# Kernel optimization log

Measured on AMD Instinct MI355X. Metric: run time of the kernel, lower is better.

## Reference

```python
import jax, jax.numpy as jnp
import numpy as np

B, T, C = 4, 2048, 1024
H = 16
HD = C // H


def setup_inputs() -> dict:
    key = jax.random.key(0)
    k1, k2, k3 = jax.random.split(key, 3)
    x = jax.random.normal(k1, (B, T, C), dtype=jnp.float32)
    w_qkv = jax.random.normal(k2, (C, 3 * C), dtype=jnp.float32) * (C ** -0.5)
    w_proj = jax.random.normal(k3, (C, C), dtype=jnp.float32) * (C ** -0.5)
    b_proj = jnp.zeros((C,), dtype=jnp.float32)
    return {"x": x, "w_qkv": w_qkv, "w_proj": w_proj, "b_proj": b_proj}


def reference(x, w_qkv, w_proj, b_proj):
    Bd, Td, Cd = x.shape
    scale = HD ** -0.5
    qkv = x @ w_qkv  # [B,T,3C]
    q, k, v = jnp.split(qkv, 3, axis=-1)
    # [B,H,T,HD]
    q = q.reshape(Bd, Td, H, HD).transpose(0, 2, 1, 3)
    k = k.reshape(Bd, Td, H, HD).transpose(0, 2, 1, 3)
    v = v.reshape(Bd, Td, H, HD).transpose(0, 2, 1, 3)
    att = jnp.einsum('bhqd,bhkd->bhqk', q, k) * scale
    causal = jnp.triu(jnp.ones((Td, Td), dtype=bool), k=1)
    att = jnp.where(causal, -jnp.inf, att)
    att = jax.nn.softmax(att, axis=-1)
    y = jnp.einsum('bhqk,bhkd->bhqd', att, v)
    y = y.transpose(0, 2, 1, 3).reshape(Bd, Td, Cd)
    return y @ w_proj + b_proj
```

## Files before the change

kernel.cpp:

```cpp
#include <hip/hip_runtime.h>

typedef unsigned short u16;
typedef __attribute__((ext_vector_type(8))) short short8;
typedef __attribute__((ext_vector_type(4))) short short4v;
typedef __attribute__((ext_vector_type(4))) float floatx4;
typedef __attribute__((ext_vector_type(4))) unsigned short ushort4v;

#define B_ 4
#define T_ 2048
#define C_ 1024
#define H_ 16
#define HD_ 64

template <bool V> struct BC { static constexpr bool value = V; };
template <int N> struct ICN { static constexpr int v = N; };

static __device__ __forceinline__ u16 f2bf(float f) {
  union { float f; unsigned int i; } c; c.f = f;
  unsigned int u = c.i;
  return (u16)((u + 0x7FFFu + ((u >> 16) & 1u)) >> 16);
}
static __device__ __forceinline__ unsigned pk2(float lo, float hi) {
  union { float f; unsigned u; } a, b; a.f = hi; b.f = lo;
  return __builtin_amdgcn_perm(a.u, b.u, 0x07060302u);
}
static __device__ __forceinline__ unsigned pk2r(float lo, float hi) {
  return (unsigned)f2bf(lo) | ((unsigned)f2bf(hi) << 16);
}

static __device__ __forceinline__ void gload16(const u16* g, u16* l) {
  __builtin_amdgcn_global_load_lds(
      (const __attribute__((address_space(1))) unsigned int*)(g),
      (__attribute__((address_space(3))) unsigned int*)(l), 16, 0, 0);
}

template <int N> static __device__ __forceinline__ void wait_vm_bar() {
  if constexpr (N == 6)
    asm volatile("s_waitcnt vmcnt(6)\n\ts_barrier" ::: "memory");
  else if constexpr (N == 4)
    asm volatile("s_waitcnt vmcnt(4)\n\ts_barrier" ::: "memory");
  else if constexpr (N == 0)
    asm volatile("s_waitcnt vmcnt(0)\n\ts_barrier" ::: "memory");
}

__global__ __launch_bounds__(256) void prep_k(const float* __restrict__ x,
                                              const float* __restrict__ w_qkv,
                                              const float* __restrict__ w_proj,
                                              u16* __restrict__ xbf,
                                              u16* __restrict__ wqkvT,
                                              u16* __restrict__ wprojT) {
  const int bid = blockIdx.x;
  if (bid < 8192) {
    const int i = bid * 256 + threadIdx.x;
    const float4 f = ((const float4*)x)[i];
    ushort4v o;
    o.x = f2bf(f.x); o.y = f2bf(f.y); o.z = f2bf(f.z); o.w = f2bf(f.w);
    *(ushort4v*)(xbf + (size_t)i * 4) = o;
    return;
  }
  __shared__ u16 tile[32][33];
  const float* in;
  u16* out;
  int R, Cc, tb;
  if (bid < 11264) {
    in = w_qkv; out = wqkvT; R = C_; Cc = 3 * C_; tb = bid - 8192;
  } else {
    in = w_proj; out = wprojT; R = C_; Cc = C_; tb = bid - 11264;
  }
  const int tpr = Cc / 32;
  const int bx = (tb % tpr) * 32;
  const int by = (tb / tpr) * 32;
  const int tx = threadIdx.x & 31;
  const int ty = threadIdx.x >> 5;
  #pragma unroll
  for (int i = ty; i < 32; i += 8)
    tile[i][tx] = f2bf(in[(size_t)(by + i) * Cc + bx + tx]);
  __syncthreads();
  #pragma unroll
  for (int i = ty; i < 32; i += 8)
    out[(size_t)(bx + i) * R + by + tx] = tile[tx][i];
}

template <int MODE, int NFR>
__global__ __launch_bounds__(256, 2) void gemm4w(const u16* __restrict__ A,
                                                 const u16* __restrict__ Bt,
                                                 u16* __restrict__ outb,
                                                 u16* __restrict__ outv,
                                                 float* __restrict__ outf,
                                                 const float* __restrict__ bias,
                                                 int M, int N) {
  constexpr int TN = NFR * 32;
  constexpr int BUFA = 4096;
  constexpr int BUFB = TN * 32;
  constexpr int BUF = BUFA + BUFB;
  constexpr int LPW = (8 + TN / 16) / 4;
  __shared__ __align__(16) u16 lds[3 * BUF];

  const int bid = blockIdx.x;
  const int xcd = bid & 7;
  const int loc = bid >> 3;
  const int tM = (xcd * 8 + (loc & 7)) * 128;
  const int tN = (loc >> 3) * TN;
  const int tid = threadIdx.x;
  const int wave = tid >> 6;
  const int lane = tid & 63;
  const int lr = lane & 15;
  const int quad = lane >> 4;
  const int wm = wave >> 1;
  const int wn = wave & 1;
  const int csw = (lr >> 1) & 3;
  const int srow = lane >> 2;
  const int skofs = ((lane & 3) ^ ((lane >> 3) & 3)) * 8;

  const u16* gbase[LPW];
  int ldst[LPW];
  #pragma unroll
  for (int j = 0; j < LPW; j++) {
    const int s = wave * LPW + j;
    if (s < 8) {
      gbase[j] = A + (size_t)(tM + s * 16 + srow) * 1024 + skofs;
      ldst[j] = s * 512;
    } else {
      gbase[j] = Bt + (size_t)(tN + (s - 8) * 16 + srow) * 1024 + skofs;
      ldst[j] = BUFA + (s - 8) * 512;
    }
  }

  const floatx4 zf = {0.f, 0.f, 0.f, 0.f};
  floatx4 acc[4][NFR];
  #pragma unroll
  for (int i = 0; i < 4; i++)
    #pragma unroll
    for (int j = 0; j < NFR; j++) acc[i][j] = zf;

  auto stage = [&](int t, int buf) {
    #pragma unroll
    for (int j = 0; j < LPW; j++)
      gload16(gbase[j] + t * 32, &lds[buf * BUF + ldst[j]]);
  };

  auto ktile = [&](int t, int buf, auto VM) {
    constexpr int vm = decltype(VM)::v;
    const u16* lA = &lds[buf * BUF];
    const u16* lB = lA + BUFA;
    short8 af[4], bfr[NFR];
    #pragma unroll
    for (int mt = 0; mt < 4; mt++)
      af[mt] = *(const short8*)(&lA[(wm * 64 + mt * 16 + lr) * 32 + ((quad ^ csw) * 8)]);
    #pragma unroll
    for (int nt = 0; nt < NFR; nt++)
      bfr[nt] = *(const short8*)(&lB[(wn * (NFR * 16) + nt * 16 + lr) * 32 + ((quad ^ csw) * 8)]);
    if constexpr (vm > 0) stage(t + 2, (buf + 2) % 3);
    __builtin_amdgcn_s_setprio(1);
    #pragma unroll
    for (int mt = 0; mt < 4; mt++)
      #pragma unroll
      for (int nt = 0; nt < NFR; nt++)
        acc[mt][nt] = __builtin_amdgcn_mfma_f32_16x16x32_bf16(af[mt], bfr[nt],
                                                              acc[mt][nt], 0, 0, 0);
    __builtin_amdgcn_s_setprio(0);
    if constexpr (vm > 0) wait_vm_bar<LPW>();
    else if constexpr (vm == 0) wait_vm_bar<0>();
  };

  stage(0, 0); stage(1, 1);
  wait_vm_bar<LPW>();

  for (int tb = 0; tb < 10; ++tb) {
    const int t = tb * 3;
    ktile(t,     0, ICN<LPW>{});
    ktile(t + 1, 1, ICN<LPW>{});
    ktile(t + 2, 2, ICN<LPW>{});
  }
  ktile(30, 0, ICN<0>{});
  ktile(31, 1, ICN<-1>{});

  if constexpr (MODE == 1) {
    if (tN >= 2 * C_) {
      asm volatile("s_barrier" ::: "memory");
      #pragma unroll
      for (int mt = 0; mt < 4; mt++) {
        const int t0 = wm * 64 + mt * 16 + quad * 4;
        #pragma unroll
        for (int nt = 0; nt < NFR; nt++) {
          const int vrow = wn * (NFR * 16) + nt * 16 + lr;
          u16* p = &lds[vrow * 128 + (((t0 >> 3) ^ (vrow & 7)) * 8) + (t0 & 7)];
          *(unsigned*)(p)     = pk2r(acc[mt][nt][0], acc[mt][nt][1]);
          *(unsigned*)(p + 2) = pk2r(acc[mt][nt][2], acc[mt][nt][3]);
        }
      }
      asm volatile("s_waitcnt lgkmcnt(0)\n\ts_barrier" ::: "memory");
      const int b = tM >> 11;
      const int t0b = tM & (T_ - 1);
      const int h0 = (tN - 2 * C_) >> 6;
      u16* vb = outv + (size_t)(b * H_ + h0) * HD_ * T_;
      #pragma unroll
      for (int i = 0; i < 16; i++) {
        const int lin = tid + i * 256;
        const int row = lin >> 4;
        const int chv = lin & 15;
        const short8 v = *(const short8*)(&lds[row * 128 + ((chv ^ (row & 7)) * 8)]);
        *(short8*)(vb + (size_t)row * T_ + t0b + chv * 8) = v;
      }
      return;
    }
    #pragma unroll
    for (int mt = 0; mt < 4; mt++) {
      const int m0 = tM + wm * 64 + mt * 16 + quad * 4;
      #pragma unroll
      for (int nt = 0; nt < NFR; nt++) {
        const int n = tN + wn * (NFR * 16) + nt * 16 + lr;
        #pragma unroll
        for (int r = 0; r < 4; r++)
          outb[(size_t)(m0 + r) * N + n] = f2bf(acc[mt][nt][r]);
      }
    }
  } else {
    #pragma unroll
    for (int mt = 0; mt < 4; mt++) {
      const int m0 = tM + wm * 64 + mt * 16 + quad * 4;
      #pragma unroll
      for (int nt = 0; nt < NFR; nt++) {
        const int n = tN + wn * (NFR * 16) + nt * 16 + lr;
        const float bv = bias[n];
        #pragma unroll
        for (int r = 0; r < 4; r++)
          __builtin_nontemporal_store(acc[mt][nt][r] + bv,
                                      &outf[(size_t)(m0 + r) * N + n]);
      }
    }
  }
}

__global__ __launch_bounds__(256, 4) void attn_k(const u16* __restrict__ qkv,
                                                 const u16* __restrict__ vt,
                                                 u16* __restrict__ y) {
  __shared__ __align__(16) u16 Ks[64 * 64];
  __shared__ __align__(16) u16 Vs[64 * 64];
  const int bid = blockIdx.x;
  const int s = bid >> 3;
  const int qp = s >> 3;
  const int bh = ((s & 7) << 3) | (bid & 7);
  const int b = bh >> 4, h = bh & 15;
  const int tid = threadIdx.x;
  const int wave = tid >> 6;
  const int lane = tid & 63;
  const int lr = lane & 15;
  const int quad = lane >> 4;
  const int qtA = qp, qtB = 31 - qp;

  const int srow = lane >> 3;
  const int skofs = ((lane & 7) ^ ((lane >> 3) & 7)) * 8;
  const int gsw = lr & 7;

  const size_t RS = 3 * C_;
  const u16* qcol = qkv + (size_t)b * T_ * RS + h * HD_;
  const u16* kcol = qcol + C_;

  const size_t qrA = (size_t)(qtA * 64 + wave * 16 + lr) * RS;
  const size_t qrB = (size_t)(qtB * 64 + wave * 16 + lr) * RS;
  const short8 aq0A = *(const short8*)(qcol + qrA + quad * 8);
  const short8 aq1A = *(const short8*)(qcol + qrA + 32 + quad * 8);
  const short8 aq0B = *(const short8*)(qcol + qrB + quad * 8);
  const short8 aq1B = *(const short8*)(qcol + qrB + 32 + quad * 8);

  const floatx4 zf = {0.f, 0.f, 0.f, 0.f};
  const float C1 = 0.125f * 1.44269504f;
  const float C2 = -16.0f * 1.44269504f;
  const short8 vones = {16256, 16256, 16256, 16256, 16256, 16256, 16256, 16256};

  floatx4 accA[4], accB[4];
  floatx4 accSA = zf, accSB = zf;
  #pragma unroll
  for (int i = 0; i < 4; i++) { accA[i] = zf; accB[i] = zf; }

  auto stage = [&](int kt) {
    __syncthreads();
    #pragma unroll
    for (int j = 0; j < 2; j++) {
      const int seg = wave * 2 + j;
      const int row = seg * 8 + srow;
      gload16(kcol + (size_t)(kt * 64 + row) * RS + skofs, &Ks[seg * 512]);
      gload16(vt + ((size_t)bh * HD_ + row) * T_ + kt * 64 + skofs, &Vs[seg * 512]);
    }
    __syncthreads();
  };

  auto core = [&](auto WA, auto DA, auto DB) {
    constexpr bool wA = decltype(WA)::value;
    constexpr bool dA = decltype(DA)::value;
    constexpr bool dB = decltype(DB)::value;
    float peA[4][4], peB[4][4];
    #pragma unroll
    for (int nt = 0; nt < 4; nt++) {
      const short8 bk0 =
          *(const short8*)(&Ks[(nt * 16 + lr) * 64 + ((quad ^ gsw) * 8)]);
      const short8 bk1 =
          *(const short8*)(&Ks[(nt * 16 + lr) * 64 + (((quad + 4) ^ gsw) * 8)]);
      {
        floatx4 st = __builtin_amdgcn_mfma_f32_16x16x32_bf16(
            bk1, aq1B,
            __builtin_amdgcn_mfma_f32_16x16x32_bf16(bk0, aq0B, zf, 0, 0, 0),
            0, 0, 0);
        #pragma unroll
        for (int r = 0; r < 4; r++) {
          float pe = __builtin_amdgcn_exp2f(fmaf(st[r], C1, C2));
          if constexpr (dB)
            if (nt * 16 + quad * 4 + r > wave * 16 + lr) pe = 0.f;
          peB[nt][r] = pe;
        }
      }
      if constexpr (wA) {
        floatx4 st = __builtin_amdgcn_mfma_f32_16x16x32_bf16(
            bk1, aq1A,
            __builtin_amdgcn_mfma_f32_16x16x32_bf16(bk0, aq0A, zf, 0, 0, 0),
            0, 0, 0);
        #pragma unroll
        for (int r = 0; r < 4; r++) {
          float pe = __builtin_amdgcn_exp2f(fmaf(st[r], C1, C2));
          if constexpr (dA)
            if (nt * 16 + quad * 4 + r > wave * 16 + lr) pe = 0.f;
          peA[nt][r] = pe;
        }
      }
    }

    short8 pB[2], pA[2];
    #pragma unroll
    for (int h2 = 0; h2 < 2; h2++) {
      union { unsigned u[4]; short8 s8; } w;
      w.u[0] = pk2(peB[2 * h2][0], peB[2 * h2][1]);
      w.u[1] = pk2(peB[2 * h2][2], peB[2 * h2][3]);
      w.u[2] = pk2(peB[2 * h2 + 1][0], peB[2 * h2 + 1][1]);
      w.u[3] = pk2(peB[2 * h2 + 1][2], peB[2 * h2 + 1][3]);
      pB[h2] = w.s8;
    }
    if constexpr (wA) {
      #pragma unroll
      for (int h2 = 0; h2 < 2; h2++) {
        union { unsigned u[4]; short8 s8; } w;
        w.u[0] = pk2(peA[2 * h2][0], peA[2 * h2][1]);
        w.u[1] = pk2(peA[2 * h2][2], peA[2 * h2][3]);
        w.u[2] = pk2(peA[2 * h2 + 1][0], peA[2 * h2 + 1][1]);
        w.u[3] = pk2(peA[2 * h2 + 1][2], peA[2 * h2 + 1][3]);
        pA[h2] = w.s8;
      }
    }

    #pragma unroll
    for (int h2 = 0; h2 < 2; h2++) {
      accSB = __builtin_amdgcn_mfma_f32_16x16x32_bf16(vones, pB[h2], accSB, 0, 0, 0);
      if constexpr (wA)
        accSA = __builtin_amdgcn_mfma_f32_16x16x32_bf16(vones, pA[h2], accSA, 0, 0, 0);
      #pragma unroll
      for (int dt = 0; dt < 4; dt++) {
        const int base = (dt * 16 + lr) * 64;
        const int cl = h2 * 4 + (quad >> 1);
        const int off_lo = ((cl ^ gsw) * 8) + (quad & 1) * 4;
        const int off_hi = (((cl + 2) ^ gsw) * 8) + (quad & 1) * 4;
        const short4v vlo = *(const short4v*)(&Vs[base + off_lo]);
        const short4v vhi = *(const short4v*)(&Vs[base + off_hi]);
        const short8 av = __builtin_shufflevector(vlo, vhi, 0, 1, 2, 3, 4, 5, 6, 7);
        accB[dt] = __builtin_amdgcn_mfma_f32_16x16x32_bf16(av, pB[h2], accB[dt], 0, 0, 0);
        if constexpr (wA)
          accA[dt] = __builtin_amdgcn_mfma_f32_16x16x32_bf16(av, pA[h2], accA[dt], 0, 0, 0);
      }
    }
  };

  for (int kt = 0; kt < qtA; kt++) { stage(kt); core(BC<true>{}, BC<false>{}, BC<false>{}); }
  stage(qtA); core(BC<true>{}, BC<true>{}, BC<false>{});
  for (int kt = qtA + 1; kt < qtB; kt++) { stage(kt); core(BC<false>{}, BC<false>{}, BC<false>{}); }
  stage(qtB); core(BC<false>{}, BC<false>{}, BC<true>{});

  #pragma unroll
  for (int ph = 0; ph < 2; ph++) {
    const int qt = ph ? qtB : qtA;
    const floatx4* acc = ph ? accB : accA;
    const float inv = 1.f / (ph ? accSB[0] : accSA[0]);
    const int qg = qt * 64 + wave * 16 + lr;
    u16* yrow = y + ((size_t)(b * T_ + qg)) * C_ + h * HD_;
    #pragma unroll
    for (int dt = 0; dt < 4; dt++) {
      ushort4v o;
      #pragma unroll
      for (int r = 0; r < 4; r++) o[r] = f2bf(acc[dt][r] * inv);
      *(ushort4v*)(yrow + dt * 16 + quad * 4) = o;
    }
  }
}

extern "C" void kernel_launch(void* const* d_in, const int* in_sizes, int n_in,
                              void* d_out, int out_size, void* d_ws, size_t ws_size,
                              hipStream_t stream) {
  const float* x      = (const float*)d_in[0];
  const float* w_qkv  = (const float*)d_in[1];
  const float* w_proj = (const float*)d_in[2];
  const float* b_proj = (const float*)d_in[3];
  float* out = (float*)d_out;

  u16* ws = (u16*)d_ws;
  const size_t SZ = (size_t)B_ * T_ * C_;
  u16* xbf    = ws;
  u16* wqkvT  = xbf + SZ;
  u16* wprojT = wqkvT + (size_t)3 * C_ * C_;
  u16* qkvw   = wprojT + (size_t)C_ * C_;
  u16* vtw    = qkvw + 3 * SZ;
  u16* yw     = xbf;

  prep_k<<<12288, 256, 0, stream>>>(x, w_qkv, w_proj, xbf, wqkvT, wprojT);
  gemm4w<1, 8><<<768, 256, 0, stream>>>(
      xbf, wqkvT, qkvw, vtw, nullptr, nullptr, B_ * T_, 3 * C_);
  attn_k<<<1024, 256, 0, stream>>>(qkvw, vtw, yw);
  gemm4w<2, 4><<<512, 256, 0, stream>>>(
      yw, wprojT, nullptr, nullptr, out, b_proj, B_ * T_, C_);
}
```

Baseline: 229.7 us.

## Deepen GEMM pipeline to 4 LDS stages with register double-buffered fragments

Replaces the 3-buffer LDS ring in the bf16 MFMA GEMM with a 4-buffer ring that keeps three tiles in flight. Operand fragments are double-buffered in registers, so the LDS reads for the next k-tile are issued before the MFMAs of the current one, with sched_barrier keeping that order. This is meant to hide LDS read latency and global-load latency behind MFMA work. In exchange, the QKV GEMM now uses launch_bounds of 1 block per CU and needs more LDS and registers, so occupancy drops and latency hiding across blocks is lost.

Result: slower. 254.6 us (+10.8%).

```diff
diff --git a/kernel.cpp b/kernel.cpp
--- a/kernel.cpp
+++ b/kernel.cpp
@@ -13,7 +13,6 @@
 #define HD_ 64
 
 template <bool V> struct BC { static constexpr bool value = V; };
-template <int N> struct ICN { static constexpr int v = N; };
 
 static __device__ __forceinline__ u16 f2bf(float f) {
   union { float f; unsigned int i; } c; c.f = f;
@@ -82,19 +81,20 @@
 }
 
 template <int MODE, int NFR>
-__global__ __launch_bounds__(256, 2) void gemm4w(const u16* __restrict__ A,
-                                                 const u16* __restrict__ Bt,
-                                                 u16* __restrict__ outb,
-                                                 u16* __restrict__ outv,
-                                                 float* __restrict__ outf,
-                                                 const float* __restrict__ bias,
-                                                 int M, int N) {
+__global__ __launch_bounds__(256, MODE == 1 ? 1 : 2)
+void gemmpf(const u16* __restrict__ A,
+            const u16* __restrict__ Bt,
+            u16* __restrict__ outb,
+            u16* __restrict__ outv,
+            float* __restrict__ outf,
+            const float* __restrict__ bias,
+            int M, int N) {
   constexpr int TN = NFR * 32;
   constexpr int BUFA = 4096;
   constexpr int BUFB = TN * 32;
   constexpr int BUF = BUFA + BUFB;
   constexpr int LPW = (8 + TN / 16) / 4;
-  __shared__ __align__(16) u16 lds[3 * BUF];
+  __shared__ __align__(16) u16 lds[4 * BUF];
 
   const int bid = blockIdx.x;
   const int xcd = bid & 7;
@@ -133,47 +133,67 @@
     #pragma unroll
     for (int j = 0; j < NFR; j++) acc[i][j] = zf;
 
-  auto stage = [&](int t, int buf) {
+  auto stage = [&](int t) {
+    const int buf = t & 3;
     #pragma unroll
     for (int j = 0; j < LPW; j++)
       gload16(gbase[j] + t * 32, &lds[buf * BUF + ldst[j]]);
   };
 
-  auto ktile = [&](int t, int buf, auto VM) {
-    constexpr int vm = decltype(VM)::v;
-    const u16* lA = &lds[buf * BUF];
+  auto readf = [&](int t, short8 (&af)[4], short8 (&bf)[NFR]) {
+    const u16* lA = &lds[(t & 3) * BUF];
     const u16* lB = lA + BUFA;
-    short8 af[4], bfr[NFR];
     #pragma unroll
     for (int mt = 0; mt < 4; mt++)
       af[mt] = *(const short8*)(&lA[(wm * 64 + mt * 16 + lr) * 32 + ((quad ^ csw) * 8)]);
     #pragma unroll
     for (int nt = 0; nt < NFR; nt++)
-      bfr[nt] = *(const short8*)(&lB[(wn * (NFR * 16) + nt * 16 + lr) * 32 + ((quad ^ csw) * 8)]);
-    if constexpr (vm > 0) stage(t + 2, (buf + 2) % 3);
+      bf[nt] = *(const short8*)(&lB[(wn * (NFR * 16) + nt * 16 + lr) * 32 + ((quad ^ csw) * 8)]);
+  };
+
+  auto domfma = [&](short8 (&af)[4], short8 (&bf)[NFR]) {
     __builtin_amdgcn_s_setprio(1);
     #pragma unroll
     for (int mt = 0; mt < 4; mt++)
       #pragma unroll
       for (int nt = 0; nt < NFR; nt++)
-        acc[mt][nt] = __builtin_amdgcn_mfma_f32_16x16x32_bf16(af[mt], bfr[nt],
+        acc[mt][nt] = __builtin_amdgcn_mfma_f32_16x16x32_bf16(af[mt], bf[nt],
                                                               acc[mt][nt], 0, 0, 0);
     __builtin_amdgcn_s_setprio(0);
-    if constexpr (vm > 0) wait_vm_bar<LPW>();
-    else if constexpr (vm == 0) wait_vm_bar<0>();
   };
 
-  stage(0, 0); stage(1, 1);
+  short8 af0[4], bf0[NFR], af1[4], bf1[NFR];
+
+  stage(0); stage(1); stage(2);
   wait_vm_bar<LPW>();
-
-  for (int tb = 0; tb < 10; ++tb) {
-    const int t = tb * 3;
-    ktile(t,     0, ICN<LPW>{});
-    ktile(t + 1, 1, ICN<LPW>{});
-    ktile(t + 2, 2, ICN<LPW>{});
-  }
-  ktile(30, 0, ICN<0>{});
-  ktile(31, 1, ICN<-1>{});
+  readf(0, af0, bf0);
+
+  #pragma unroll 1
+  for (int tb = 0; tb < 14; tb++) {
+    const int t = 2 * tb;
+    readf(t + 1, af1, bf1);
+    stage(t + 3);
+    __builtin_amdgcn_sched_barrier(0);
+    domfma(af0, bf0);
+    wait_vm_bar<LPW>();
+    readf(t + 2, af0, bf0);
+    stage(t + 4);
+    __builtin_amdgcn_sched_barrier(0);
+    domfma(af1, bf1);
+    wait_vm_bar<LPW>();
+  }
+  readf(29, af1, bf1); stage(31);
+  __builtin_amdgcn_sched_barrier(0);
+  domfma(af0, bf0);
+  wait_vm_bar<LPW>();
+  readf(30, af0, bf0);
+  __builtin_amdgcn_sched_barrier(0);
+  domfma(af1, bf1);
+  wait_vm_bar<0>();
+  readf(31, af1, bf1);
+  __builtin_amdgcn_sched_barrier(0);
+  domfma(af0, bf0);
+  domfma(af1, bf1);
 
   if constexpr (MODE == 1) {
     if (tN >= 2 * C_) {
@@ -409,9 +429,9 @@
   u16* yw     = xbf;
 
   prep_k<<<12288, 256, 0, stream>>>(x, w_qkv, w_proj, xbf, wqkvT, wprojT);
-  gemm4w<1, 8><<<768, 256, 0, stream>>>(
+  gemmpf<1, 8><<<768, 256, 0, stream>>>(
       xbf, wqkvT, qkvw, vtw, nullptr, nullptr, B_ * T_, 3 * C_);
   attn_k<<<1024, 256, 0, stream>>>(qkvw, vtw, yw);
-  gemm4w<2, 4><<<512, 256, 0, stream>>>(
+  gemmpf<2, 4><<<512, 256, 0, stream>>>(
       yw, wprojT, nullptr, nullptr, out, b_proj, B_ * T_, C_);
 }
```

## Double-buffer K/V tiles in attention to overlap loads with MFMA compute

Applied to the files above, without the earlier changes.

Doubles the shared K and V tiles into two buffers and prefetches the next key tile while computing on the current one. The two __syncthreads per iteration are replaced by a single waitcnt+barrier after compute. The aim is to hide global-to-LDS load latency behind the MFMA work. LDS use rises from 16KB to 32KB per block, which could cut occupancy at the 4-blocks-per-CU launch bound.

Result: no change. 231.9 us (+0.9%).

```diff
diff --git a/kernel.cpp b/kernel.cpp
--- a/kernel.cpp
+++ b/kernel.cpp
@@ -235,8 +235,8 @@
 __global__ __launch_bounds__(256, 4) void attn_k(const u16* __restrict__ qkv,
                                                  const u16* __restrict__ vt,
                                                  u16* __restrict__ y) {
-  __shared__ __align__(16) u16 Ks[64 * 64];
-  __shared__ __align__(16) u16 Vs[64 * 64];
+  __shared__ __align__(16) u16 Ks[2 * 4096];
+  __shared__ __align__(16) u16 Vs[2 * 4096];
   const int bid = blockIdx.x;
   const int s = bid >> 3;
   const int qp = s >> 3;
@@ -274,29 +274,30 @@
   #pragma unroll
   for (int i = 0; i < 4; i++) { accA[i] = zf; accB[i] = zf; }
 
-  auto stage = [&](int kt) {
-    __syncthreads();
+  auto stage = [&](int kt, int buf) {
     #pragma unroll
     for (int j = 0; j < 2; j++) {
       const int seg = wave * 2 + j;
       const int row = seg * 8 + srow;
-      gload16(kcol + (size_t)(kt * 64 + row) * RS + skofs, &Ks[seg * 512]);
-      gload16(vt + ((size_t)bh * HD_ + row) * T_ + kt * 64 + skofs, &Vs[seg * 512]);
-    }
-    __syncthreads();
+      gload16(kcol + (size_t)(kt * 64 + row) * RS + skofs, &Ks[buf * 4096 + seg * 512]);
+      gload16(vt + ((size_t)bh * HD_ + row) * T_ + kt * 64 + skofs, &Vs[buf * 4096 + seg * 512]);
+    }
+    __builtin_amdgcn_sched_barrier(0);
   };
 
-  auto core = [&](auto WA, auto DA, auto DB) {
+  auto core = [&](int cur, auto WA, auto DA, auto DB) {
     constexpr bool wA = decltype(WA)::value;
     constexpr bool dA = decltype(DA)::value;
     constexpr bool dB = decltype(DB)::value;
+    const u16* Kb = &Ks[cur * 4096];
+    const u16* Vb = &Vs[cur * 4096];
     float peA[4][4], peB[4][4];
     #pragma unroll
     for (int nt = 0; nt < 4; nt++) {
       const short8 bk0 =
-          *(const short8*)(&Ks[(nt * 16 + lr) * 64 + ((quad ^ gsw) * 8)]);
+          *(const short8*)(&Kb[(nt * 16 + lr) * 64 + ((quad ^ gsw) * 8)]);
       const short8 bk1 =
-          *(const short8*)(&Ks[(nt * 16 + lr) * 64 + (((quad + 4) ^ gsw) * 8)]);
+          *(const short8*)(&Kb[(nt * 16 + lr) * 64 + (((quad + 4) ^ gsw) * 8)]);
       {
         floatx4 st = __builtin_amdgcn_mfma_f32_16x16x32_bf16(
             bk1, aq1B,
@@ -358,8 +359,8 @@
         const int cl = h2 * 4 + (quad >> 1);
         const int off_lo = ((cl ^ gsw) * 8) + (quad & 1) * 4;
         const int off_hi = (((cl + 2) ^ gsw) * 8) + (quad & 1) * 4;
-        const short4v vlo = *(const short4v*)(&Vs[base + off_lo]);
-        const short4v vhi = *(const short4v*)(&Vs[base + off_hi]);
+        const short4v vlo = *(const short4v*)(&Vb[base + off_lo]);
+        const short4v vhi = *(const short4v*)(&Vb[base + off_hi]);
         const short8 av = __builtin_shufflevector(vlo, vhi, 0, 1, 2, 3, 4, 5, 6, 7);
         accB[dt] = __builtin_amdgcn_mfma_f32_16x16x32_bf16(av, pB[h2], accB[dt], 0, 0, 0);
         if constexpr (wA)
@@ -368,10 +369,26 @@
     }
   };
 
-  for (int kt = 0; kt < qtA; kt++) { stage(kt); core(BC<true>{}, BC<false>{}, BC<false>{}); }
-  stage(qtA); core(BC<true>{}, BC<true>{}, BC<false>{});
-  for (int kt = qtA + 1; kt < qtB; kt++) { stage(kt); core(BC<false>{}, BC<false>{}, BC<false>{}); }
-  stage(qtB); core(BC<false>{}, BC<false>{}, BC<true>{});
+  stage(0, 0);
+  asm volatile("s_waitcnt vmcnt(0)\n\ts_barrier" ::: "memory");
+  int cur = 0;
+  for (int kt = 0; kt < qtA; kt++) {
+    stage(kt + 1, cur ^ 1);
+    core(cur, BC<true>{}, BC<false>{}, BC<false>{});
+    asm volatile("s_waitcnt vmcnt(0)\n\ts_barrier" ::: "memory");
+    cur ^= 1;
+  }
+  stage(qtA + 1, cur ^ 1);
+  core(cur, BC<true>{}, BC<true>{}, BC<false>{});
+  asm volatile("s_waitcnt vmcnt(0)\n\ts_barrier" ::: "memory");
+  cur ^= 1;
+  for (int kt = qtA + 1; kt < qtB; kt++) {
+    stage(kt + 1, cur ^ 1);
+    core(cur, BC<false>{}, BC<false>{}, BC<false>{});
+    asm volatile("s_waitcnt vmcnt(0)\n\ts_barrier" ::: "memory");
+    cur ^= 1;
+  }
+  core(cur, BC<false>{}, BC<false>{}, BC<true>{});
 
   #pragma unroll
   for (int ph = 0; ph < 2; ph++) {
```
